# Optimization experiments

Hardware: AMD Instinct MI355X
Metric: run time of the kernel (lower is better)

## Reference

```python
import jax, jax.numpy as jnp
import numpy as np

B, L, H, M = 8, 512, 768, 383
N = M + 1  # +1 dummy epsilon mention
NEG = -10000.0


def _lin(x, W, b):
    return x @ W.T + b


def setup_inputs() -> dict:
    key = jax.random.key(0)
    ks = jax.random.split(key, 26)
    s = 0.02
    inp = {}
    inp["sequence_output"] = jax.random.normal(ks[0], (B, L, H), jnp.float32)
    inp["speaker_emb"] = jax.random.normal(ks[1], (400, H), jnp.float32) * s
    inp["dummy_emb"] = jax.random.normal(ks[2], (1, H), jnp.float32) * s
    inp["W_pair1"] = jax.random.normal(ks[3], (H, 2 * H), jnp.float32) * s
    inp["b_pair1"] = jnp.zeros((H,), jnp.float32)
    inp["W_pair2"] = jax.random.normal(ks[4], (H // 2, H), jnp.float32) * s
    inp["b_pair2"] = jnp.zeros((H // 2,), jnp.float32)
    inp["W_pair3"] = jax.random.normal(ks[5], (1, H // 2), jnp.float32) * s
    inp["b_pair3"] = jnp.zeros((1,), jnp.float32)
    inp["W_m1"] = jax.random.normal(ks[6], (H // 2, H), jnp.float32) * s
    inp["b_m1"] = jnp.zeros((H // 2,), jnp.float32)
    inp["W_m2"] = jax.random.normal(ks[7], (H // 4, H // 2), jnp.float32) * s
    inp["b_m2"] = jnp.zeros((H // 4,), jnp.float32)
    inp["W_m3"] = jax.random.normal(ks[8], (1, H // 4), jnp.float32) * s
    inp["b_m3"] = jnp.zeros((1,), jnp.float32)
    inp["W_c1"] = jax.random.normal(ks[9], (H // 2, H), jnp.float32) * s
    inp["b_c1"] = jnp.zeros((H // 2,), jnp.float32)
    inp["W_c2"] = jax.random.normal(ks[10], (18, H // 2), jnp.float32) * s
    inp["b_c2"] = jnp.zeros((18,), jnp.float32)
    inp["mentions_seg"] = jax.random.randint(ks[11], (M,), 0, B, jnp.int32)
    inp["mention_start"] = jax.random.randint(ks[12], (M,), 0, L, jnp.int32)
    inp["mention_end"] = jax.random.randint(ks[13], (M,), 0, L, jnp.int32)
    inp["speaker_ids"] = jax.random.randint(ks[14], (B, L), 0, 400, jnp.int32)
    second = jnp.arange(1, N, dtype=jnp.int32)  # each real mention is a 'second' exactly once
    first = jax.random.randint(ks[15], (M,), 0, N, jnp.int32) % second  # antecedent strictly before
    inp["link_first"] = first
    inp["link_second"] = second
    inp["character_label"] = jax.random.randint(ks[16], (M,), 0, 18, jnp.int32)
    return inp


def reference(sequence_output, speaker_emb, dummy_emb,
              W_pair1, b_pair1, W_pair2, b_pair2, W_pair3, b_pair3,
              W_m1, b_m1, W_m2, b_m2, W_m3, b_m3,
              W_c1, b_c1, W_c2, b_c2,
              mentions_seg, mention_start, mention_end, speaker_ids,
              link_first, link_second, character_label):
    relu = jax.nn.relu
    # gather mention boundary + speaker reps: [M, H]
    start_rep = sequence_output[mentions_seg, mention_start]
    end_rep = sequence_output[mentions_seg, mention_end]
    spk_rep = speaker_emb[speaker_ids[mentions_seg, mention_start]]
    mention_reps = start_rep + end_rep + spk_rep
    # character linking head: [M, 18]
    char_logits = _lin(relu(_lin(mention_reps, W_c1, b_c1)), W_c2, b_c2)
    # prepend dummy epsilon mention: [N, H]
    all_reps = jnp.concatenate([dummy_emb, mention_reps], axis=0)
    # pairwise MLP; pair[i, j] = MLP(cat(rep_j, rep_i)). Split W_pair1 to avoid [N,N,2H] concat.
    Wa, Wb = W_pair1[:, :H], W_pair1[:, H:]
    A = all_reps @ Wa.T  # contribution of 'first' (column j)
    Bm = all_reps @ Wb.T  # contribution of 'second' (row i)
    h1 = relu(A[None, :, :] + Bm[:, None, :] + b_pair1)  # [N, N, H]
    h2 = relu(jnp.einsum('ijk,hk->ijh', h1, W_pair2) + b_pair2)  # [N, N, H/2]
    pair_scores = jnp.einsum('ijh,oh->ij', h2, W_pair3) + b_pair3[0]  # [N, N]
    # unary mention score: [N]
    ms = (_lin(relu(_lin(relu(_lin(all_reps, W_m1, b_m1)), W_m2, b_m2)), W_m3, b_m3))[:, 0]
    mask = jnp.triu(jnp.ones((N, N), jnp.float32), k=0) * NEG
    mention_scores = pair_scores + ms[None, :] + ms[:, None] + mask
    # linking loss via row-softmax and link gathers
    sm = jax.nn.softmax(mention_scores, axis=1)
    lik = sm[link_second, link_first]  # [num_links]
    col_sum = jnp.zeros((N,), sm.dtype).at[link_second].add(lik)
    nll = -jnp.sum(jnp.log(col_sum[1:]))
    # character cross-entropy (sum reduction)
    logp = jax.nn.log_softmax(char_logits, axis=1)
    ce = -jnp.sum(jnp.take_along_axis(logp, character_label[:, None], axis=1))
    return nll + ce


if __name__ == '__main__':
    out = reference(**setup_inputs())
    print(out)
```

## Files before the change

kernel.cpp:

```cpp
#include <hip/hip_runtime.h>

typedef __bf16 bf16x8 __attribute__((ext_vector_type(8)));
typedef float f32x4 __attribute__((ext_vector_type(4)));

#define WS_ALLREPS 0
#define WS_APRIME  294912
#define WS_BMAT    589824
#define WS_RELUM1  884736
#define WS_RELUC1  1032192
#define WS_MS      1179648
#define WS_SSUM    1180032
#define WS_PF      1180416
#define WS_W2BF    1180800

#define SWZ(row,c) (((row)<<2) + ((c) ^ (((row)>>1)&3)))

__device__ __forceinline__ bf16x8 cvt8(float4 a, float4 b) {
  bf16x8 v;
  v[0]=(__bf16)a.x; v[1]=(__bf16)a.y; v[2]=(__bf16)a.z; v[3]=(__bf16)a.w;
  v[4]=(__bf16)b.x; v[5]=(__bf16)b.y; v[6]=(__bf16)b.z; v[7]=(__bf16)b.w;
  return v;
}

__global__ __launch_bounds__(256) void k_build(
    const float* __restrict__ seq, const float* __restrict__ spk_emb,
    const float* __restrict__ dummy, const float* __restrict__ W2,
    const int* __restrict__ seg, const int* __restrict__ mstart,
    const int* __restrict__ mend, const int* __restrict__ spk_ids,
    float* __restrict__ all_reps, __bf16* __restrict__ W2bf) {
  int r = blockIdx.x, t = threadIdx.x;
  if (r < 384) {
    if (r == 0) {
      #pragma unroll
      for (int e = 0; e < 3; ++e) { int k = t + 256*e; all_reps[k] = dummy[k]; }
    } else {
      int m = r - 1;
      int sg = seg[m], st = mstart[m], en = mend[m];
      int sp = spk_ids[sg*512 + st];
      const float* p1 = seq + (size_t)(sg*512 + st)*768;
      const float* p2 = seq + (size_t)(sg*512 + en)*768;
      const float* p3 = spk_emb + (size_t)sp*768;
      #pragma unroll
      for (int e = 0; e < 3; ++e) { int k = t + 256*e; all_reps[r*768+k] = p1[k]+p2[k]+p3[k]; }
    }
  } else {
    int h = r - 384;
    #pragma unroll
    for (int e = 0; e < 3; ++e) { int k = t + 256*e; W2bf[h*768+k] = (__bf16)W2[h*768+k]; }
  }
}

__global__ __launch_bounds__(256) void k_gemmB(
    const float* __restrict__ reps, const float* __restrict__ W1,
    const float* __restrict__ Wm1, const float* __restrict__ Wc1,
    const float* __restrict__ b1, const float* __restrict__ bm1, const float* __restrict__ bc1,
    float* __restrict__ Aprime, float* __restrict__ Bmat,
    float* __restrict__ relu_m1, float* __restrict__ relu_c1) {
  __shared__ bf16x8 lA[256];
  __shared__ bf16x8 lB[512];
  int nt = blockIdx.x;
  int m0 = blockIdx.y * 64;
  int t = threadIdx.x;
  const float* src; int stride, coloff;
  if (nt < 6)       { src = W1  + (size_t)(nt*128)*1536;      stride = 1536; coloff = 0;   }
  else if (nt < 12) { src = W1  + (size_t)((nt-6)*128)*1536;  stride = 1536; coloff = 768; }
  else if (nt < 15) { src = Wm1 + (size_t)((nt-12)*128)*768;  stride = 768;  coloff = 0;   }
  else              { src = Wc1 + (size_t)((nt-15)*128)*768;  stride = 768;  coloff = 0;   }

  int w = t>>6, l = t&63;
  int wm = w&1, wn = w>>1;
  int lr = l&15, lg = l>>4;

  int p = t>>2, q = t&3;
  const float* pa  = reps + (size_t)(m0+p)*768 + q*8;
  const float* pb0 = src + (size_t)p*stride + coloff + q*8;
  const float* pb1 = src + (size_t)(p+64)*stride + coloff + q*8;
  int ia  = SWZ(p, q);
  int ib0 = SWZ(p, q);
  int ib1 = SWZ(p+64, q);

  f32x4 acc[2][4] = {};

  for (int ks = 0; ks < 24; ++ks) {
    int k0 = ks*32;
    float4 a0 = *(const float4*)(pa + k0);
    float4 a1 = *(const float4*)(pa + k0 + 4);
    float4 b0 = *(const float4*)(pb0 + k0);
    float4 b1v = *(const float4*)(pb0 + k0 + 4);
    float4 c0 = *(const float4*)(pb1 + k0);
    float4 c1v = *(const float4*)(pb1 + k0 + 4);
    lA[ia]  = cvt8(a0, a1);
    lB[ib0] = cvt8(b0, b1v);
    lB[ib1] = cvt8(c0, c1v);
    __syncthreads();
    bf16x8 af[2], bfr[4];
    #pragma unroll
    for (int fa = 0; fa < 2; ++fa) { int row = wm*32 + fa*16 + lr; af[fa] = lA[SWZ(row, lg)]; }
    #pragma unroll
    for (int fb = 0; fb < 4; ++fb) { int row = wn*64 + fb*16 + lr; bfr[fb] = lB[SWZ(row, lg)]; }
    #pragma unroll
    for (int fa = 0; fa < 2; ++fa)
      #pragma unroll
      for (int fb = 0; fb < 4; ++fb)
        acc[fa][fb] = __builtin_amdgcn_mfma_f32_16x16x32_bf16(af[fa], bfr[fb], acc[fa][fb], 0, 0, 0);
    __syncthreads();
  }

  #pragma unroll
  for (int fa = 0; fa < 2; ++fa) {
    #pragma unroll
    for (int fb = 0; fb < 4; ++fb) {
      #pragma unroll
      for (int reg = 0; reg < 4; ++reg) {
        int m = m0 + wm*32 + fa*16 + lg*4 + reg;
        int nl = wn*64 + fb*16 + lr;
        float v = acc[fa][fb][reg];
        if (nt < 6)       { int n = nt*128 + nl;      Aprime[m*768+n]  = v + b1[n]; }
        else if (nt < 12) { int n = (nt-6)*128 + nl;  Bmat[m*768+n]    = v; }
        else if (nt < 15) { int n = (nt-12)*128 + nl; relu_m1[m*384+n] = fmaxf(v + bm1[n], 0.f); }
        else              { int n = (nt-15)*128 + nl; relu_c1[m*384+n] = fmaxf(v + bc1[n], 0.f); }
      }
    }
  }
}

__global__ __launch_bounds__(192) void k_ms(
    const float* __restrict__ relu_m1, const float* __restrict__ Wm2,
    const float* __restrict__ bm2, const float* __restrict__ Wm3,
    const float* __restrict__ bm3, float* __restrict__ ms) {
  __shared__ float x[8][384];
  __shared__ float part[8][3];
  int r0 = blockIdx.x*8, t = threadIdx.x;
  const float4* srcv = (const float4*)(relu_m1 + (size_t)r0*384);
  float4* dstv = (float4*)&x[0][0];
  #pragma unroll
  for (int e = 0; e < 4; ++e) dstv[t + 192*e] = srcv[t + 192*e];
  __syncthreads();
  float a[8] = {};
  const float4* wv = (const float4*)(Wm2 + (size_t)t*384);
  for (int k = 0; k < 96; ++k) {
    float4 wq = wv[k];
    #pragma unroll
    for (int r = 0; r < 8; ++r) {
      float4 xq = *(const float4*)&x[r][k*4];
      a[r] += wq.x*xq.x + wq.y*xq.y + wq.z*xq.z + wq.w*xq.w;
    }
  }
  float wm3 = Wm3[t], bb = bm2[t];
  #pragma unroll
  for (int r = 0; r < 8; ++r) {
    float c = fmaxf(a[r] + bb, 0.f) * wm3;
    c += __shfl_xor(c, 1);  c += __shfl_xor(c, 2);  c += __shfl_xor(c, 4);
    c += __shfl_xor(c, 8);  c += __shfl_xor(c, 16); c += __shfl_xor(c, 32);
    if ((t&63) == 0) part[r][t>>6] = c;
  }
  __syncthreads();
  if (t < 8) ms[r0+t] = part[t][0] + part[t][1] + part[t][2] + bm3[0];
}

__global__ __launch_bounds__(512) void k_pair(
    const float* __restrict__ Aprime, const float* __restrict__ Bmat,
    const __bf16* __restrict__ W2bf, const float* __restrict__ b2,
    const float* __restrict__ w3, const float* __restrict__ b3,
    const float* __restrict__ ms, const int* __restrict__ lfirst,
    float* __restrict__ Ssum, float* __restrict__ Pf) {
  int bid = blockIdx.x;
  int ib = (int)((__fsqrt_rn(4.0f*bid + 1.0f) - 1.0f) * 0.5f);
  while ((ib+1)*(ib+2) <= bid) ++ib;
  while (ib*(ib+1) > bid) --ib;
  int jb = bid - ib*(ib+1);
  int i0 = ib*16, j0 = jb*8;

  __shared__ bf16x8 lA[2][512];
  __shared__ bf16x8 lB[2][1536];
  __shared__ float score_lds[128][4];

  int t = threadIdx.x;
  int w = t>>6, l = t&63;
  int wp = w&1, wh = w>>1;
  int lr = l&15, lg = l>>4;

  int p = t>>2, q = t&3;
  const float* pArow = Aprime + (size_t)(j0 + (p&7))*768 + q*8;
  const float* pBrow = Bmat   + (size_t)(i0 + (p>>3))*768 + q*8;
  const __bf16* pW0 = W2bf + (size_t)p*768       + q*8;
  const __bf16* pW1 = W2bf + (size_t)(p+128)*768 + q*8;
  const __bf16* pW2p = W2bf + (size_t)(p+256)*768 + q*8;
  int idxH  = SWZ(p, q);
  int idxW0 = SWZ(p, q);
  int idxW1 = SWZ(p+128, q);
  int idxW2 = SWZ(p+256, q);

  float4 ga0, ga1, gb0, gb1;
  bf16x8 gw0, gw1, gw2;

  #define LOADG(k0) { \
    ga0 = *(const float4*)(pArow + (k0)); \
    ga1 = *(const float4*)(pArow + (k0) + 4); \
    gb0 = *(const float4*)(pBrow + (k0)); \
    gb1 = *(const float4*)(pBrow + (k0) + 4); \
    gw0 = *(const bf16x8*)(pW0  + (k0)); \
    gw1 = *(const bf16x8*)(pW1  + (k0)); \
    gw2 = *(const bf16x8*)(pW2p + (k0)); }

  #define WRITEB(buf) { \
    float4 r0, r1; \
    r0.x = fmaxf(ga0.x + gb0.x, 0.f); r0.y = fmaxf(ga0.y + gb0.y, 0.f); \
    r0.z = fmaxf(ga0.z + gb0.z, 0.f); r0.w = fmaxf(ga0.w + gb0.w, 0.f); \
    r1.x = fmaxf(ga1.x + gb1.x, 0.f); r1.y = fmaxf(ga1.y + gb1.y, 0.f); \
    r1.z = fmaxf(ga1.z + gb1.z, 0.f); r1.w = fmaxf(ga1.w + gb1.w, 0.f); \
    lA[buf][idxH]  = cvt8(r0, r1); \
    lB[buf][idxW0] = gw0; lB[buf][idxW1] = gw1; lB[buf][idxW2] = gw2; }

  LOADG(0);
  WRITEB(0);

  f32x4 acc[4][6] = {};
  int cur = 0;

  for (int ks = 0; ks < 24; ++ks) {
    __syncthreads();
    if (ks < 23) LOADG((ks+1)*32);
    bf16x8 af[4], bfr[6];
    #pragma unroll
    for (int fp = 0; fp < 4; ++fp) { int row = wp*64 + fp*16 + lr; af[fp] = lA[cur][SWZ(row, lg)]; }
    #pragma unroll
    for (int fh = 0; fh < 6; ++fh) { int row = wh*96 + fh*16 + lr; bfr[fh] = lB[cur][SWZ(row, lg)]; }
    __builtin_amdgcn_s_setprio(1);
    #pragma unroll
    for (int fp = 0; fp < 4; ++fp)
      #pragma unroll
      for (int fh = 0; fh < 6; ++fh)
        acc[fp][fh] = __builtin_amdgcn_mfma_f32_16x16x32_bf16(af[fp], bfr[fh], acc[fp][fh], 0, 0, 0);
    __builtin_amdgcn_s_setprio(0);
    if (ks < 23) WRITEB(cur^1);
    cur ^= 1;
  }

  float sacc[4][4] = {};
  #pragma unroll
  for (int fh = 0; fh < 6; ++fh) {
    int hcol = wh*96 + fh*16 + lr;
    float bb = b2[hcol], ww = w3[hcol];
    #pragma unroll
    for (int fp = 0; fp < 4; ++fp)
      #pragma unroll
      for (int reg = 0; reg < 4; ++reg)
        sacc[fp][reg] += fmaxf(acc[fp][fh][reg] + bb, 0.f) * ww;
  }
  #pragma unroll
  for (int fp = 0; fp < 4; ++fp) {
    #pragma unroll
    for (int reg = 0; reg < 4; ++reg) {
      float v = sacc[fp][reg];
      v += __shfl_xor(v, 1); v += __shfl_xor(v, 2);
      v += __shfl_xor(v, 4); v += __shfl_xor(v, 8);
      if (lr == 0) score_lds[wp*64 + fp*16 + lg*4 + reg][wh] = v;
    }
  }
  __syncthreads();

  if (t < 128) {
    int pp = t;
    float s = score_lds[pp][0] + score_lds[pp][1] + score_lds[pp][2] + score_lds[pp][3] + b3[0];
    int i = i0 + (pp>>3), j = j0 + (pp&7);
    float e = 0.f;
    if (j < i) {
      float sm = s + ms[j];
      e = __expf(sm);
      if (j == lfirst[i-1]) Pf[i] = sm;
    }
    e += __shfl_xor(e, 1); e += __shfl_xor(e, 2); e += __shfl_xor(e, 4);
    if ((t&7) == 0) atomicAdd(&Ssum[i], e);
  }
}

__global__ __launch_bounds__(64) void k_ce(
    const float* __restrict__ relu_c1, const float* __restrict__ Wc2,
    const float* __restrict__ bc2, const int* __restrict__ label,
    float* __restrict__ out) {
  __shared__ float lg[18];
  int m = blockIdx.x, t = threadIdx.x;
  if (t < 18) {
    const float4* xv = (const float4*)(relu_c1 + (size_t)(m+1)*384);
    const float4* wv = (const float4*)(Wc2 + (size_t)t*384);
    float d = 0.f;
    for (int k = 0; k < 96; ++k) {
      float4 a = xv[k], b = wv[k];
      d += a.x*b.x + a.y*b.y + a.z*b.z + a.w*b.w;
    }
    lg[t] = d + bc2[t];
  }
  __syncthreads();
  if (t == 0) {
    float sum = 0.f;
    for (int c = 0; c < 18; ++c) sum += __expf(lg[c]);
    atomicAdd(out, __logf(sum) - lg[label[m]]);
  }
}

__global__ __launch_bounds__(384) void k_nll(
    const float* __restrict__ Ssum, const float* __restrict__ Pf,
    float* __restrict__ out) {
  int i = threadIdx.x;
  if (i >= 1) atomicAdd(out, __logf(Ssum[i]) - Pf[i]);
}

extern "C" void kernel_launch(void* const* d_in, const int* in_sizes, int n_in,
                              void* d_out, int out_size, void* d_ws, size_t ws_size,
                              hipStream_t stream) {
  (void)in_sizes; (void)n_in; (void)out_size; (void)ws_size;
  const float* seq   = (const float*)d_in[0];
  const float* spk   = (const float*)d_in[1];
  const float* dummy = (const float*)d_in[2];
  const float* W1    = (const float*)d_in[3];
  const float* b1    = (const float*)d_in[4];
  const float* W2    = (const float*)d_in[5];
  const float* b2    = (const float*)d_in[6];
  const float* W3    = (const float*)d_in[7];
  const float* b3    = (const float*)d_in[8];
  const float* Wm1   = (const float*)d_in[9];
  const float* bm1   = (const float*)d_in[10];
  const float* Wm2   = (const float*)d_in[11];
  const float* bm2   = (const float*)d_in[12];
  const float* Wm3   = (const float*)d_in[13];
  const float* bm3   = (const float*)d_in[14];
  const float* Wc1   = (const float*)d_in[15];
  const float* bc1   = (const float*)d_in[16];
  const float* Wc2   = (const float*)d_in[17];
  const float* bc2   = (const float*)d_in[18];
  const int* seg     = (const int*)d_in[19];
  const int* mstart  = (const int*)d_in[20];
  const int* mend    = (const int*)d_in[21];
  const int* spk_ids = (const int*)d_in[22];
  const int* lfirst  = (const int*)d_in[23];
  const int* clabel  = (const int*)d_in[25];

  float* ws = (float*)d_ws;
  float* all_reps = ws + WS_ALLREPS;
  float* Aprime   = ws + WS_APRIME;
  float* Bmat     = ws + WS_BMAT;
  float* relu_m1  = ws + WS_RELUM1;
  float* relu_c1  = ws + WS_RELUC1;
  float* msv      = ws + WS_MS;
  float* Ssum     = ws + WS_SSUM;
  float* Pf       = ws + WS_PF;
  __bf16* W2bf    = (__bf16*)(ws + WS_W2BF);
  float* out      = (float*)d_out;

  hipMemsetAsync(out, 0, sizeof(float), stream);
  hipMemsetAsync(Ssum, 0, 384*sizeof(float), stream);

  k_build<<<768, 256, 0, stream>>>(seq, spk, dummy, W2, seg, mstart, mend, spk_ids, all_reps, W2bf);
  k_gemmB<<<dim3(18,6), 256, 0, stream>>>(all_reps, W1, Wm1, Wc1, b1, bm1, bc1, Aprime, Bmat, relu_m1, relu_c1);
  k_ms<<<48, 192, 0, stream>>>(relu_m1, Wm2, bm2, Wm3, bm3, msv);
  k_pair<<<600, 512, 0, stream>>>(Aprime, Bmat, W2bf, b2, W3, b3, msv, lfirst, Ssum, Pf);
  k_ce<<<383, 64, 0, stream>>>(relu_c1, Wc2, bc2, clabel, out);
  k_nll<<<1, 384, 0, stream>>>(Ssum, Pf, out);
}
```

Measured before the change: 261.2 us.

## Split pair kernel over hidden halves, double-buffer gemmB, move softmax to epilogue

Splits the pair-scoring kernel along the hidden dimension into two 256-thread blocks per tile, each writing partial scores to a workspace buffer, so twice as many smaller blocks can run with two blocks per CU. The exp/sum/link-gather logic moves into a new per-row epilogue kernel, which drops the per-element atomics and the Ssum memset. The output memset is also removed, with out now zeroed inside k_build. k_gemmB gets double-buffered LDS with register prefetch and MFMA priority hints, and k_ms uses more, smaller blocks. The cost is an extra partial-score write and read through global memory, an extra launch, and duplicated A/B relu work across the two hidden halves.

```diff
diff --git a/kernel.cpp b/kernel.cpp
--- a/kernel.cpp
+++ b/kernel.cpp
@@ -9,9 +9,8 @@
 #define WS_RELUM1  884736
 #define WS_RELUC1  1032192
 #define WS_MS      1179648
-#define WS_SSUM    1180032
-#define WS_PF      1180416
-#define WS_W2BF    1180800
+#define WS_W2BF    1180032
+#define WS_S       1327488
 
 #define SWZ(row,c) (((row)<<2) + ((c) ^ (((row)>>1)&3)))
 
@@ -27,10 +26,12 @@
     const float* __restrict__ dummy, const float* __restrict__ W2,
     const int* __restrict__ seg, const int* __restrict__ mstart,
     const int* __restrict__ mend, const int* __restrict__ spk_ids,
-    float* __restrict__ all_reps, __bf16* __restrict__ W2bf) {
+    float* __restrict__ all_reps, __bf16* __restrict__ W2bf,
+    float* __restrict__ out) {
   int r = blockIdx.x, t = threadIdx.x;
   if (r < 384) {
     if (r == 0) {
+      if (t == 0) out[0] = 0.f;
       #pragma unroll
       for (int e = 0; e < 3; ++e) { int k = t + 256*e; all_reps[k] = dummy[k]; }
     } else {
@@ -56,8 +57,8 @@
     const float* __restrict__ b1, const float* __restrict__ bm1, const float* __restrict__ bc1,
     float* __restrict__ Aprime, float* __restrict__ Bmat,
     float* __restrict__ relu_m1, float* __restrict__ relu_c1) {
-  __shared__ bf16x8 lA[256];
-  __shared__ bf16x8 lB[512];
+  __shared__ bf16x8 lA[2][256];
+  __shared__ bf16x8 lB[2][512];
   int nt = blockIdx.x;
   int m0 = blockIdx.y * 64;
   int t = threadIdx.x;
@@ -79,31 +80,39 @@
   int ib0 = SWZ(p, q);
   int ib1 = SWZ(p+64, q);
 
+  float4 a0, a1, b0, b1v, c0, c1v;
+  #define G_LOADG(k0) { \
+    a0  = *(const float4*)(pa  + (k0)); a1  = *(const float4*)(pa  + (k0) + 4); \
+    b0  = *(const float4*)(pb0 + (k0)); b1v = *(const float4*)(pb0 + (k0) + 4); \
+    c0  = *(const float4*)(pb1 + (k0)); c1v = *(const float4*)(pb1 + (k0) + 4); }
+  #define G_WRITEB(buf) { \
+    lA[buf][ia]  = cvt8(a0, a1); \
+    lB[buf][ib0] = cvt8(b0, b1v); \
+    lB[buf][ib1] = cvt8(c0, c1v); }
+
+  G_LOADG(0);
+  G_WRITEB(0);
+
   f32x4 acc[2][4] = {};
+  int cur = 0;
 
   for (int ks = 0; ks < 24; ++ks) {
-    int k0 = ks*32;
-    float4 a0 = *(const float4*)(pa + k0);
-    float4 a1 = *(const float4*)(pa + k0 + 4);
-    float4 b0 = *(const float4*)(pb0 + k0);
-    float4 b1v = *(const float4*)(pb0 + k0 + 4);
-    float4 c0 = *(const float4*)(pb1 + k0);
-    float4 c1v = *(const float4*)(pb1 + k0 + 4);
-    lA[ia]  = cvt8(a0, a1);
-    lB[ib0] = cvt8(b0, b1v);
-    lB[ib1] = cvt8(c0, c1v);
     __syncthreads();
+    if (ks < 23) G_LOADG((ks+1)*32);
     bf16x8 af[2], bfr[4];
     #pragma unroll
-    for (int fa = 0; fa < 2; ++fa) { int row = wm*32 + fa*16 + lr; af[fa] = lA[SWZ(row, lg)]; }
-    #pragma unroll
-    for (int fb = 0; fb < 4; ++fb) { int row = wn*64 + fb*16 + lr; bfr[fb] = lB[SWZ(row, lg)]; }
+    for (int fa = 0; fa < 2; ++fa) { int row = wm*32 + fa*16 + lr; af[fa] = lA[cur][SWZ(row, lg)]; }
+    #pragma unroll
+    for (int fb = 0; fb < 4; ++fb) { int row = wn*64 + fb*16 + lr; bfr[fb] = lB[cur][SWZ(row, lg)]; }
+    __builtin_amdgcn_s_setprio(1);
     #pragma unroll
     for (int fa = 0; fa < 2; ++fa)
       #pragma unroll
       for (int fb = 0; fb < 4; ++fb)
         acc[fa][fb] = __builtin_amdgcn_mfma_f32_16x16x32_bf16(af[fa], bfr[fb], acc[fa][fb], 0, 0, 0);
-    __syncthreads();
+    __builtin_amdgcn_s_setprio(0);
+    if (ks < 23) G_WRITEB(cur^1);
+    cur ^= 1;
   }
 
   #pragma unroll
@@ -128,43 +137,43 @@
     const float* __restrict__ relu_m1, const float* __restrict__ Wm2,
     const float* __restrict__ bm2, const float* __restrict__ Wm3,
     const float* __restrict__ bm3, float* __restrict__ ms) {
-  __shared__ float x[8][384];
-  __shared__ float part[8][3];
-  int r0 = blockIdx.x*8, t = threadIdx.x;
+  __shared__ float x[2][384];
+  __shared__ float part[2][3];
+  int r0 = blockIdx.x*2, t = threadIdx.x;
   const float4* srcv = (const float4*)(relu_m1 + (size_t)r0*384);
   float4* dstv = (float4*)&x[0][0];
-  #pragma unroll
-  for (int e = 0; e < 4; ++e) dstv[t + 192*e] = srcv[t + 192*e];
+  dstv[t] = srcv[t];
   __syncthreads();
-  float a[8] = {};
+  float a[2] = {};
   const float4* wv = (const float4*)(Wm2 + (size_t)t*384);
   for (int k = 0; k < 96; ++k) {
     float4 wq = wv[k];
     #pragma unroll
-    for (int r = 0; r < 8; ++r) {
+    for (int r = 0; r < 2; ++r) {
       float4 xq = *(const float4*)&x[r][k*4];
       a[r] += wq.x*xq.x + wq.y*xq.y + wq.z*xq.z + wq.w*xq.w;
     }
   }
   float wm3 = Wm3[t], bb = bm2[t];
   #pragma unroll
-  for (int r = 0; r < 8; ++r) {
+  for (int r = 0; r < 2; ++r) {
     float c = fmaxf(a[r] + bb, 0.f) * wm3;
     c += __shfl_xor(c, 1);  c += __shfl_xor(c, 2);  c += __shfl_xor(c, 4);
     c += __shfl_xor(c, 8);  c += __shfl_xor(c, 16); c += __shfl_xor(c, 32);
     if ((t&63) == 0) part[r][t>>6] = c;
   }
   __syncthreads();
-  if (t < 8) ms[r0+t] = part[t][0] + part[t][1] + part[t][2] + bm3[0];
-}
-
-__global__ __launch_bounds__(512) void k_pair(
+  if (t < 2) ms[r0+t] = part[t][0] + part[t][1] + part[t][2] + bm3[0];
+}
+
+__global__ __launch_bounds__(256, 2) void k_pair(
     const float* __restrict__ Aprime, const float* __restrict__ Bmat,
     const __bf16* __restrict__ W2bf, const float* __restrict__ b2,
-    const float* __restrict__ w3, const float* __restrict__ b3,
-    const float* __restrict__ ms, const int* __restrict__ lfirst,
-    float* __restrict__ Ssum, float* __restrict__ Pf) {
+    const float* __restrict__ w3,
+    float* __restrict__ S) {
   int bid = blockIdx.x;
+  int hh = blockIdx.y;
+  int h0 = hh * 192;
   int ib = (int)((__fsqrt_rn(4.0f*bid + 1.0f) - 1.0f) * 0.5f);
   while ((ib+1)*(ib+2) <= bid) ++ib;
   while (ib*(ib+1) > bid) --ib;
@@ -172,45 +181,51 @@
   int i0 = ib*16, j0 = jb*8;
 
   __shared__ bf16x8 lA[2][512];
-  __shared__ bf16x8 lB[2][1536];
-  __shared__ float score_lds[128][4];
+  __shared__ bf16x8 lB[2][768];
+  __shared__ float score_lds[128][2];
 
   int t = threadIdx.x;
   int w = t>>6, l = t&63;
   int wp = w&1, wh = w>>1;
   int lr = l&15, lg = l>>4;
 
-  int p = t>>2, q = t&3;
-  const float* pArow = Aprime + (size_t)(j0 + (p&7))*768 + q*8;
-  const float* pBrow = Bmat   + (size_t)(i0 + (p>>3))*768 + q*8;
-  const __bf16* pW0 = W2bf + (size_t)p*768       + q*8;
-  const __bf16* pW1 = W2bf + (size_t)(p+128)*768 + q*8;
-  const __bf16* pW2p = W2bf + (size_t)(p+256)*768 + q*8;
-  int idxH  = SWZ(p, q);
-  int idxW0 = SWZ(p, q);
-  int idxW1 = SWZ(p+128, q);
-  int idxW2 = SWZ(p+256, q);
-
-  float4 ga0, ga1, gb0, gb1;
+  int p = t>>1, qb = (t&1)*2;
+  const float* pArow = Aprime + (size_t)(j0 + (p&7))*768 + qb*8;
+  const float* pBrow = Bmat   + (size_t)(i0 + (p>>3))*768 + qb*8;
+  int idxA0 = SWZ(p, qb), idxA1 = SWZ(p, qb+1);
+  const __bf16* pW[3]; int idxW[3];
+  #pragma unroll
+  for (int e = 0; e < 3; ++e) {
+    int c = t + 256*e, row = c>>2, qq = c&3;
+    pW[e] = W2bf + (size_t)(h0 + row)*768 + qq*8;
+    idxW[e] = SWZ(row, qq);
+  }
+
+  float4 ga0, ga1, ga2, ga3, gb0, gb1, gb2, gb3;
   bf16x8 gw0, gw1, gw2;
 
   #define LOADG(k0) { \
-    ga0 = *(const float4*)(pArow + (k0)); \
-    ga1 = *(const float4*)(pArow + (k0) + 4); \
-    gb0 = *(const float4*)(pBrow + (k0)); \
-    gb1 = *(const float4*)(pBrow + (k0) + 4); \
-    gw0 = *(const bf16x8*)(pW0  + (k0)); \
-    gw1 = *(const bf16x8*)(pW1  + (k0)); \
-    gw2 = *(const bf16x8*)(pW2p + (k0)); }
+    ga0 = *(const float4*)(pArow + (k0));     ga1 = *(const float4*)(pArow + (k0) + 4); \
+    ga2 = *(const float4*)(pArow + (k0) + 8); ga3 = *(const float4*)(pArow + (k0) + 12); \
+    gb0 = *(const float4*)(pBrow + (k0));     gb1 = *(const float4*)(pBrow + (k0) + 4); \
+    gb2 = *(const float4*)(pBrow + (k0) + 8); gb3 = *(const float4*)(pBrow + (k0) + 12); \
+    gw0 = *(const bf16x8*)(pW[0] + (k0)); \
+    gw1 = *(const bf16x8*)(pW[1] + (k0)); \
+    gw2 = *(const bf16x8*)(pW[2] + (k0)); }
 
   #define WRITEB(buf) { \
-    float4 r0, r1; \
+    float4 r0, r1, r2, r3; \
     r0.x = fmaxf(ga0.x + gb0.x, 0.f); r0.y = fmaxf(ga0.y + gb0.y, 0.f); \
     r0.z = fmaxf(ga0.z + gb0.z, 0.f); r0.w = fmaxf(ga0.w + gb0.w, 0.f); \
     r1.x = fmaxf(ga1.x + gb1.x, 0.f); r1.y = fmaxf(ga1.y + gb1.y, 0.f); \
     r1.z = fmaxf(ga1.z + gb1.z, 0.f); r1.w = fmaxf(ga1.w + gb1.w, 0.f); \
-    lA[buf][idxH]  = cvt8(r0, r1); \
-    lB[buf][idxW0] = gw0; lB[buf][idxW1] = gw1; lB[buf][idxW2] = gw2; }
+    r2.x = fmaxf(ga2.x + gb2.x, 0.f); r2.y = fmaxf(ga2.y + gb2.y, 0.f); \
+    r2.z = fmaxf(ga2.z + gb2.z, 0.f); r2.w = fmaxf(ga2.w + gb2.w, 0.f); \
+    r3.x = fmaxf(ga3.x + gb3.x, 0.f); r3.y = fmaxf(ga3.y + gb3.y, 0.f); \
+    r3.z = fmaxf(ga3.z + gb3.z, 0.f); r3.w = fmaxf(ga3.w + gb3.w, 0.f); \
+    lA[buf][idxA0] = cvt8(r0, r1); \
+    lA[buf][idxA1] = cvt8(r2, r3); \
+    lB[buf][idxW[0]] = gw0; lB[buf][idxW[1]] = gw1; lB[buf][idxW[2]] = gw2; }
 
   LOADG(0);
   WRITEB(0);
@@ -240,7 +255,7 @@
   float sacc[4][4] = {};
   #pragma unroll
   for (int fh = 0; fh < 6; ++fh) {
-    int hcol = wh*96 + fh*16 + lr;
+    int hcol = h0 + wh*96 + fh*16 + lr;
     float bb = b2[hcol], ww = w3[hcol];
     #pragma unroll
     for (int fp = 0; fp < 4; ++fp)
@@ -259,19 +274,8 @@
     }
   }
   __syncthreads();
-
   if (t < 128) {
-    int pp = t;
-    float s = score_lds[pp][0] + score_lds[pp][1] + score_lds[pp][2] + score_lds[pp][3] + b3[0];
-    int i = i0 + (pp>>3), j = j0 + (pp&7);
-    float e = 0.f;
-    if (j < i) {
-      float sm = s + ms[j];
-      e = __expf(sm);
-      if (j == lfirst[i-1]) Pf[i] = sm;
-    }
-    e += __shfl_xor(e, 1); e += __shfl_xor(e, 2); e += __shfl_xor(e, 4);
-    if ((t&7) == 0) atomicAdd(&Ssum[i], e);
+    S[(size_t)hh*76800 + bid*128 + t] = score_lds[t][0] + score_lds[t][1];
   }
 }
 
@@ -299,11 +303,30 @@
   }
 }
 
-__global__ __launch_bounds__(384) void k_nll(
-    const float* __restrict__ Ssum, const float* __restrict__ Pf,
+__global__ __launch_bounds__(64) void k_epi(
+    const float* __restrict__ S, const float* __restrict__ ms,
+    const float* __restrict__ b3, const int* __restrict__ lfirst,
     float* __restrict__ out) {
-  int i = threadIdx.x;
-  if (i >= 1) atomicAdd(out, __logf(Ssum[i]) - Pf[i]);
+  int i = blockIdx.x + 1;
+  int lane = threadIdx.x;
+  int ibb = i >> 4, r = i & 15;
+  int f = lfirst[i-1];
+  float bb3 = b3[0];
+  float esum = 0.f, smf = 0.f;
+  for (int j = lane; j < i; j += 64) {
+    int jbb = j >> 3;
+    int idx = (ibb*(ibb+1) + jbb)*128 + r*8 + (j&7);
+    float s = S[idx] + S[76800 + idx] + bb3 + ms[j];
+    esum += __expf(s);
+    if (j == f) smf = s;
+  }
+  esum += __shfl_xor(esum, 1);  esum += __shfl_xor(esum, 2);
+  esum += __shfl_xor(esum, 4);  esum += __shfl_xor(esum, 8);
+  esum += __shfl_xor(esum, 16); esum += __shfl_xor(esum, 32);
+  smf += __shfl_xor(smf, 1);  smf += __shfl_xor(smf, 2);
+  smf += __shfl_xor(smf, 4);  smf += __shfl_xor(smf, 8);
+  smf += __shfl_xor(smf, 16); smf += __shfl_xor(smf, 32);
+  if (lane == 0) atomicAdd(out, __logf(esum) - smf);
 }
 
 extern "C" void kernel_launch(void* const* d_in, const int* in_sizes, int n_in,
@@ -343,18 +366,14 @@
   float* relu_m1  = ws + WS_RELUM1;
   float* relu_c1  = ws + WS_RELUC1;
   float* msv      = ws + WS_MS;
-  float* Ssum     = ws + WS_SSUM;
-  float* Pf       = ws + WS_PF;
   __bf16* W2bf    = (__bf16*)(ws + WS_W2BF);
+  float* S        = ws + WS_S;
   float* out      = (float*)d_out;
 
-  hipMemsetAsync(out, 0, sizeof(float), stream);
-  hipMemsetAsync(Ssum, 0, 384*sizeof(float), stream);
-
-  k_build<<<768, 256, 0, stream>>>(seq, spk, dummy, W2, seg, mstart, mend, spk_ids, all_reps, W2bf);
+  k_build<<<768, 256, 0, stream>>>(seq, spk, dummy, W2, seg, mstart, mend, spk_ids, all_reps, W2bf, out);
   k_gemmB<<<dim3(18,6), 256, 0, stream>>>(all_reps, W1, Wm1, Wc1, b1, bm1, bc1, Aprime, Bmat, relu_m1, relu_c1);
-  k_ms<<<48, 192, 0, stream>>>(relu_m1, Wm2, bm2, Wm3, bm3, msv);
-  k_pair<<<600, 512, 0, stream>>>(Aprime, Bmat, W2bf, b2, W3, b3, msv, lfirst, Ssum, Pf);
+  k_ms<<<192, 192, 0, stream>>>(relu_m1, Wm2, bm2, Wm3, bm3, msv);
+  k_pair<<<dim3(600,2), 256, 0, stream>>>(Aprime, Bmat, W2bf, b2, W3, S);
   k_ce<<<383, 64, 0, stream>>>(relu_c1, Wc2, bc2, clabel, out);
-  k_nll<<<1, 384, 0, stream>>>(Ssum, Pf, out);
-}
+  k_epi<<<383, 64, 0, stream>>>(S, msv, b3, lfirst, out);
+}
```

Result: faster. 246.8 us (-5.5%).
